# Kernel tuning notes

Measured on AMD Instinct MI355X. Metric: run time of the kernel, lower is better.

## Reference

```python
import jax, jax.numpy as jnp
import numpy as np

D_MODEL = 1024
N_HEADS = 16
D_EXP = 4
B, SQ, SKV = 2, 2048, 2048
LN_EPS = 1e-5


def _linear_params(key, d_in, d_out):
    kw, kb = jax.random.split(key)
    w = jax.random.normal(kw, (d_in, d_out), jnp.float32) * 0.02  # stored [in,out]
    b = jax.random.normal(kb, (d_out,), jnp.float32) * 0.02
    return w, b


def setup_inputs() -> dict:
    key = jax.random.key(0)
    ks = jax.random.split(key, 16)
    inp = {}
    inp["x"] = jax.random.normal(ks[0], (B, SQ, D_MODEL), jnp.float32)
    inp["encoder_out"] = jax.random.normal(ks[1], (B, SKV, D_MODEL), jnp.float32)
    # causal target mask, broadcast over batch and heads
    inp["tgt_mask"] = jnp.tril(jnp.ones((SQ, SQ), jnp.int32))[None, None]
    inp["src_mask"] = jnp.ones((1, 1, SQ, SKV), jnp.int32)
    # self-attention params
    inp["wq_s"], inp["bq_s"] = _linear_params(ks[2], D_MODEL, D_MODEL)
    inp["wk_s"], inp["bk_s"] = _linear_params(ks[3], D_MODEL, D_MODEL)
    inp["wv_s"], inp["bv_s"] = _linear_params(ks[4], D_MODEL, D_MODEL)
    inp["wo_s"], inp["bo_s"] = _linear_params(ks[5], D_MODEL, D_MODEL)
    # cross-attention params
    inp["wq_c"], inp["bq_c"] = _linear_params(ks[6], D_MODEL, D_MODEL)
    inp["wk_c"], inp["bk_c"] = _linear_params(ks[7], D_MODEL, D_MODEL)
    inp["wv_c"], inp["bv_c"] = _linear_params(ks[8], D_MODEL, D_MODEL)
    inp["wo_c"], inp["bo_c"] = _linear_params(ks[9], D_MODEL, D_MODEL)
    # feedforward params
    inp["ff1_w"], inp["ff1_b"] = _linear_params(ks[10], D_MODEL, D_MODEL * D_EXP)
    inp["ff2_w"], inp["ff2_b"] = _linear_params(ks[11], D_MODEL * D_EXP, D_MODEL)
    # layernorm params (3 AddNorms)
    for i, k in zip((1, 2, 3), (ks[12], ks[13], ks[14])):
        inp[f"ln{i}_g"] = jnp.ones((D_MODEL,), jnp.float32)
        inp[f"ln{i}_b"] = jnp.zeros((D_MODEL,), jnp.float32)
    return inp


def _layernorm(x, g, b):
    mu = jnp.mean(x, axis=-1, keepdims=True)
    var = jnp.mean(jnp.square(x - mu), axis=-1, keepdims=True)
    return (x - mu) / jnp.sqrt(var + LN_EPS) * g + b


def _mha(xq, xkv, wq, bq, wk, bk, wv, bv, wo, bo, mask):
    Bq, Sq, D = xq.shape
    Hd = D // N_HEADS
    q = (xq @ wq + bq).reshape(Bq, Sq, N_HEADS, Hd).transpose(0, 2, 1, 3)   # bhqd
    k = (xkv @ wk + bk).reshape(Bq, -1, N_HEADS, Hd).transpose(0, 2, 1, 3)  # bhkd
    v = (xkv @ wv + bv).reshape(Bq, -1, N_HEADS, Hd).transpose(0, 2, 1, 3)  # bhkd
    score = jnp.einsum("bhqd,bhkd->bhqk", q, k) / jnp.sqrt(jnp.float32(Hd))
    score = jnp.where(mask == 0, -jnp.inf, score)
    attn = jax.nn.softmax(score, axis=-1)
    ctx = jnp.einsum("bhqk,bhkd->bhqd", attn, v)
    ctx = ctx.transpose(0, 2, 1, 3).reshape(Bq, Sq, D)
    return ctx @ wo + bo


def reference(x, encoder_out, tgt_mask, src_mask,
              wq_s, bq_s, wk_s, bk_s, wv_s, bv_s, wo_s, bo_s,
              wq_c, bq_c, wk_c, bk_c, wv_c, bv_c, wo_c, bo_c,
              ff1_w, ff1_b, ff2_w, ff2_b,
              ln1_g, ln1_b, ln2_g, ln2_b, ln3_g, ln3_b):
    # dropout is identity in eval mode
    sa = _mha(x, x, wq_s, bq_s, wk_s, bk_s, wv_s, bv_s, wo_s, bo_s, tgt_mask)
    h = _layernorm(x + sa, ln1_g, ln1_b)
    ca = _mha(h, encoder_out, wq_c, bq_c, wk_c, bk_c, wv_c, bv_c, wo_c, bo_c, src_mask)
    h2 = _layernorm(h + ca, ln2_g, ln2_b)
    ff = jax.nn.relu(h2 @ ff1_w + ff1_b) @ ff2_w + ff2_b
    return _layernorm(h2 + ff, ln3_g, ln3_b)
```

## Files before the change

kernel.cpp:

```cpp
#include <hip/hip_runtime.h>
#include <stdint.h>

typedef __bf16 bf16;
typedef __attribute__((ext_vector_type(4))) float f32x4;
typedef __attribute__((ext_vector_type(8))) __bf16 bf16x8;
typedef __attribute__((ext_vector_type(4))) __bf16 bf16x4;

#define DM   1024
#define NH   16
#define HDIM 64
#define BB   2
#define SEQ  2048
#define MR   (BB * SEQ)
#define DFF  4096
#define MEG  (1024 * 1024)

__global__ void detect_kernel(const unsigned int* __restrict__ xw,
                              int* __restrict__ flag) {
  int tid = threadIdx.x;
  int bad = 0;
  for (int i = tid; i < 4096; i += 64) {
    unsigned int w = xw[i];
    float flo = __uint_as_float((w & 0xffffu) << 16);
    if (!(fabsf(flo) < 100.f)) bad = 1;
  }
  unsigned long long m = __ballot(bad);
  if (tid == 0) *flag = (m == 0ull) ? 1 : 0;
}

__global__ __launch_bounds__(256) void cvt_big_kernel(
    const void* __restrict__ src, bf16* __restrict__ dst, int n4,
    const int* __restrict__ flag) {
  int i = blockIdx.x * 256 + threadIdx.x;
  if (i >= n4) return;
  if (*flag) {
    ((bf16x4*)dst)[i] = ((const bf16x4*)src)[i];
  } else {
    float4 v = ((const float4*)src)[i];
    bf16x4 o = {(bf16)v.x, (bf16)v.y, (bf16)v.z, (bf16)v.w};
    ((bf16x4*)dst)[i] = o;
  }
}

struct P16 { const void* p[16]; };
__global__ __launch_bounds__(256) void cvt_small_kernel(
    P16 ps, bf16* __restrict__ dstbase, const int* __restrict__ flag) {
  const int ncnt[16] = {1024,1024,1024,1024,1024,1024,1024,1024,
                        4096,1024,1024,1024,1024,1024,1024,1024};
  const int doff[16] = {0,1024,2048,3072,4096,5120,6144,7168,
                        8192,12288,13312,14336,15360,16384,17408,18432};
  int b = blockIdx.x;
  int n = ncnt[b];
  bool isbf = (*flag) != 0;
  const void* s = ps.p[b];
  bf16* d = dstbase + doff[b];
  for (int i = threadIdx.x; i * 4 < n; i += 256) {
    if (isbf) {
      ((bf16x4*)d)[i] = ((const bf16x4*)s)[i];
    } else {
      float4 v = ((const float4*)s)[i];
      bf16x4 o = {(bf16)v.x, (bf16)v.y, (bf16)v.z, (bf16)v.w};
      ((bf16x4*)d)[i] = o;
    }
  }
}

static __device__ __forceinline__ void gl_lds16(const bf16* g, bf16* l) {
  auto gp = reinterpret_cast<__attribute__((address_space(1))) unsigned int*>(
      reinterpret_cast<uintptr_t>(g));
  auto lp = reinterpret_cast<__attribute__((address_space(3))) unsigned int*>(
      (unsigned int)reinterpret_cast<uintptr_t>(l));
  __builtin_amdgcn_global_load_lds(gp, lp, 16, 0, 0);
}

struct WTB {
  const void* src[10];
  int dstoff[10];
  int K[10], N[10];
  int bstart[10];
};
__global__ __launch_bounds__(256) void wt_all_kernel(WTB wb, bf16* __restrict__ wtbase,
                                                     const int* __restrict__ flag) {
  __shared__ bf16 tile[32][33];
  int bid = blockIdx.x;
  int wi = 0;
  while (wi < 9 && bid >= wb.bstart[wi + 1]) ++wi;
  int rel = bid - wb.bstart[wi];
  int N = wb.N[wi], K = wb.K[wi];
  int nb = N >> 5;
  int n0 = (rel % nb) * 32, k0 = (rel / nb) * 32;
  const void* w = wb.src[wi];
  bf16* wt = wtbase + wb.dstoff[wi];
  bool isbf = (*flag) != 0;
  int tid = threadIdx.x;
  int tx = tid & 31, ty = tid >> 5;
#pragma unroll
  for (int i = 0; i < 4; ++i) {
    size_t idx = (size_t)(k0 + ty + i * 8) * N + n0 + tx;
    tile[ty + i * 8][tx] = isbf ? ((const bf16*)w)[idx]
                                : (bf16)(((const float*)w)[idx]);
  }
  __syncthreads();
#pragma unroll
  for (int i = 0; i < 4; ++i)
    wt[(size_t)(n0 + ty + i * 8) * K + k0 + tx] = tile[tx][ty + i * 8];
}

template <int TM>
__global__ __launch_bounds__(256) void gemm_kernel(
    const bf16* __restrict__ A, const bf16* __restrict__ Bt,
    const bf16* __restrict__ bias, bf16* __restrict__ outb,
    int M, int N, int K, int relu) {
  constexpr int NI = TM / 32;
  constexpr int WM = TM / 2;
  constexpr int CA = TM / 64;
  __shared__ alignas(16) bf16 As[TM * 32];
  __shared__ alignas(16) bf16 Bs[128 * 32];
  int tid = threadIdx.x;
  int lane = tid & 63, wv = tid >> 6;
  int quad = lane >> 4, l15 = lane & 15;
  int m0 = blockIdx.y * TM, n0 = blockIdx.x * 128;
  int wm = wv >> 1, wn = wv & 1;

  f32x4 acc[NI][4];
#pragma unroll
  for (int i = 0; i < NI; ++i)
#pragma unroll
    for (int j = 0; j < 4; ++j) acc[i][j] = (f32x4){0.f, 0.f, 0.f, 0.f};

  int sr = lane >> 2, sc = (lane & 3) * 8;
  const bf16* gA[CA];
  bf16* lA[CA];
#pragma unroll
  for (int t = 0; t < CA; ++t) {
    int ch = wv * CA + t;
    gA[t] = A + (size_t)(m0 + ch * 16 + sr) * K + sc;
    lA[t] = As + ch * 512 + lane * 8;
  }
  const bf16* gB0 = Bt + (size_t)(n0 + (wv * 2) * 16 + sr) * K + sc;
  const bf16* gB1 = Bt + (size_t)(n0 + (wv * 2 + 1) * 16 + sr) * K + sc;
  bf16* lB0 = Bs + (wv * 2) * 512 + lane * 8;
  bf16* lB1 = Bs + (wv * 2 + 1) * 512 + lane * 8;

  for (int k0 = 0; k0 < K; k0 += 32) {
#pragma unroll
    for (int t = 0; t < CA; ++t) gl_lds16(gA[t] + k0, lA[t]);
    gl_lds16(gB0 + k0, lB0);
    gl_lds16(gB1 + k0, lB1);
    __syncthreads();
    bf16x8 af[NI], bfr[4];
#pragma unroll
    for (int i = 0; i < NI; ++i)
      af[i] = *(const bf16x8*)(As + (wm * WM + i * 16 + l15) * 32 + quad * 8);
#pragma unroll
    for (int j = 0; j < 4; ++j)
      bfr[j] = *(const bf16x8*)(Bs + (wn * 64 + j * 16 + l15) * 32 + quad * 8);
#pragma unroll
    for (int i = 0; i < NI; ++i)
#pragma unroll
      for (int j = 0; j < 4; ++j)
        acc[i][j] = __builtin_amdgcn_mfma_f32_16x16x32_bf16(af[i], bfr[j],
                                                            acc[i][j], 0, 0, 0);
    __syncthreads();
  }

#pragma unroll
  for (int j = 0; j < 4; ++j) {
    int col = n0 + wn * 64 + j * 16 + l15;
    float bval = (float)bias[col];
#pragma unroll
    for (int i = 0; i < NI; ++i) {
      int rb = m0 + wm * WM + i * 16 + quad * 4;
#pragma unroll
      for (int r = 0; r < 4; ++r) {
        float v = acc[i][j][r] + bval;
        if (relu) v = fmaxf(v, 0.f);
        outb[(size_t)(rb + r) * N + col] = (bf16)v;
      }
    }
  }
}

__global__ __launch_bounds__(256) void gemm_splitk_kernel(
    const bf16* __restrict__ A, const bf16* __restrict__ Bt,
    float* __restrict__ pout, int M, int N, int KC, int Ktot) {
  __shared__ alignas(16) bf16 As[128 * 32];
  __shared__ alignas(16) bf16 Bs[128 * 32];
  int tid = threadIdx.x;
  int lane = tid & 63, wv = tid >> 6;
  int quad = lane >> 4, l15 = lane & 15;
  int m0 = blockIdx.y * 128, n0 = blockIdx.x * 128;
  int wm = wv >> 1, wn = wv & 1;
  int kb = blockIdx.z * KC;
  pout += (size_t)blockIdx.z * M * N;

  f32x4 acc[4][4];
#pragma unroll
  for (int i = 0; i < 4; ++i)
#pragma unroll
    for (int j = 0; j < 4; ++j) acc[i][j] = (f32x4){0.f, 0.f, 0.f, 0.f};

  int sr = lane >> 2, sc = (lane & 3) * 8;
  const bf16* gA0 = A + (size_t)(m0 + (wv * 2) * 16 + sr) * Ktot + sc;
  const bf16* gA1 = A + (size_t)(m0 + (wv * 2 + 1) * 16 + sr) * Ktot + sc;
  const bf16* gB0 = Bt + (size_t)(n0 + (wv * 2) * 16 + sr) * Ktot + sc;
  const bf16* gB1 = Bt + (size_t)(n0 + (wv * 2 + 1) * 16 + sr) * Ktot + sc;
  bf16* lA0 = As + (wv * 2) * 512 + lane * 8;
  bf16* lA1 = As + (wv * 2 + 1) * 512 + lane * 8;
  bf16* lB0 = Bs + (wv * 2) * 512 + lane * 8;
  bf16* lB1 = Bs + (wv * 2 + 1) * 512 + lane * 8;

  for (int k0 = kb; k0 < kb + KC; k0 += 32) {
    gl_lds16(gA0 + k0, lA0);
    gl_lds16(gA1 + k0, lA1);
    gl_lds16(gB0 + k0, lB0);
    gl_lds16(gB1 + k0, lB1);
    __syncthreads();
    bf16x8 af[4], bfr[4];
#pragma unroll
    for (int i = 0; i < 4; ++i)
      af[i] = *(const bf16x8*)(As + (wm * 64 + i * 16 + l15) * 32 + quad * 8);
#pragma unroll
    for (int j = 0; j < 4; ++j)
      bfr[j] = *(const bf16x8*)(Bs + (wn * 64 + j * 16 + l15) * 32 + quad * 8);
#pragma unroll
    for (int i = 0; i < 4; ++i)
#pragma unroll
      for (int j = 0; j < 4; ++j)
        acc[i][j] = __builtin_amdgcn_mfma_f32_16x16x32_bf16(af[i], bfr[j],
                                                            acc[i][j], 0, 0, 0);
    __syncthreads();
  }
#pragma unroll
  for (int j = 0; j < 4; ++j) {
    int col = n0 + wn * 64 + j * 16 + l15;
#pragma unroll
    for (int i = 0; i < 4; ++i) {
      int rb = m0 + wm * 64 + i * 16 + quad * 4;
#pragma unroll
      for (int r = 0; r < 4; ++r)
        pout[(size_t)(rb + r) * N + col] = acc[i][j][r];
    }
  }
}

__global__ __launch_bounds__(256) void vt_pre_kernel(
    const bf16* __restrict__ v, int vstride, bf16* __restrict__ vt, int skv) {
  __shared__ bf16 tile[32][33];
  int tid = threadIdx.x;
  int tx = tid & 31, ty = tid >> 5;
  int kv0 = blockIdx.x * 32, d0 = blockIdx.y * 32;
  int bh = blockIdx.z;
  int b = bh >> 4, h = bh & 15;
  const bf16* src = v + (size_t)b * skv * vstride + h * HDIM;
#pragma unroll
  for (int i = 0; i < 4; ++i)
    tile[ty + i * 8][tx] = src[(size_t)(kv0 + ty + i * 8) * vstride + d0 + tx];
  __syncthreads();
  bf16* dst = vt + ((size_t)bh * HDIM + d0) * skv + kv0;
#pragma unroll
  for (int i = 0; i < 4; ++i)
    dst[(size_t)(ty + i * 8) * skv + tx] = tile[tx][ty + i * 8];
}

__global__ __launch_bounds__(256) void flash4_kernel(
    const bf16* __restrict__ Q, int qstride,
    const bf16* __restrict__ Kk, int kstride,
    const bf16* __restrict__ VT, bf16* __restrict__ ctx, int skv, int causal) {
  __shared__ alignas(16) bf16 Kt[2][64 * 72];
  __shared__ alignas(16) bf16 Vt[2][64 * 72];
  __shared__ alignas(16) bf16 Pt[2][4][32 * 72];
  int tid = threadIdx.x;
  int lane = tid & 63, wv = tid >> 6, quad = lane >> 4, l15 = lane & 15;
  int qb = blockIdx.x, h = blockIdx.y, b = blockIdx.z;
  int q0 = qb * 128;
  int qw = q0 + wv * 32;

  bf16x8 qf[2][2];
  const float qsc = 0.125f * 1.44269504f;
#pragma unroll
  for (int a = 0; a < 2; ++a) {
    const bf16* qp = Q + (size_t)(b * SEQ + qw + a * 16 + l15) * qstride + h * HDIM;
    qf[a][0] = *(const bf16x8*)(qp + quad * 8);
    qf[a][1] = *(const bf16x8*)(qp + 32 + quad * 8);
#pragma unroll
    for (int j = 0; j < 8; ++j) {
      qf[a][0][j] = (bf16)((float)qf[a][0][j] * qsc);
      qf[a][1][j] = (bf16)((float)qf[a][1][j] * qsc);
    }
  }
  bf16x8 onesf;
#pragma unroll
  for (int j = 0; j < 8; ++j) onesf[j] = (l15 == 0) ? (bf16)1.0f : (bf16)0.0f;

  f32x4 o[2][4], oL[2];
#pragma unroll
  for (int a = 0; a < 2; ++a) {
    oL[a] = (f32x4){0.f, 0.f, 0.f, 0.f};
#pragma unroll
    for (int j = 0; j < 4; ++j) o[a][j] = (f32x4){0.f, 0.f, 0.f, 0.f};
  }

  int nch = causal ? (q0 + 128) / 64 : skv / 64;
  int srow = tid >> 2, sseg = (tid & 3) * 16;
  const bf16* kg = Kk + (size_t)b * skv * kstride + (size_t)srow * kstride +
                   h * HDIM + sseg;
  const bf16* vg = VT + ((size_t)(b * NH + h) * HDIM + srow) * skv + sseg;

  bf16x8 k0r = *(const bf16x8*)(kg);
  bf16x8 k1r = *(const bf16x8*)(kg + 8);
  bf16x8 v0r = *(const bf16x8*)(vg);
  bf16x8 v1r = *(const bf16x8*)(vg + 8);

  for (int c = 0; c < nch; ++c) {
    int buf = c & 1;
    int kv0 = c * 64;
    *(bf16x8*)(&Kt[buf][srow * 72 + sseg]) = k0r;
    *(bf16x8*)(&Kt[buf][srow * 72 + sseg + 8]) = k1r;
    *(bf16x8*)(&Vt[buf][srow * 72 + sseg]) = v0r;
    *(bf16x8*)(&Vt[buf][srow * 72 + sseg + 8]) = v1r;
    if (c + 1 < nch) {
      const bf16* kn = kg + (size_t)(kv0 + 64) * kstride;
      const bf16* vn = vg + kv0 + 64;
      k0r = *(const bf16x8*)(kn);
      k1r = *(const bf16x8*)(kn + 8);
      v0r = *(const bf16x8*)(vn);
      v1r = *(const bf16x8*)(vn + 8);
    }
    __syncthreads();

    if (!causal || kv0 <= qw + 31) {
      f32x4 s[2][4];
#pragma unroll
      for (int t = 0; t < 4; ++t) {
        bf16x8 kt0 = *(const bf16x8*)(&Kt[buf][(t * 16 + l15) * 72 + quad * 8]);
        bf16x8 kt1 = *(const bf16x8*)(&Kt[buf][(t * 16 + l15) * 72 + 32 + quad * 8]);
#pragma unroll
        for (int a = 0; a < 2; ++a) {
          f32x4 z = (f32x4){0.f, 0.f, 0.f, 0.f};
          z = __builtin_amdgcn_mfma_f32_16x16x32_bf16(kt0, qf[a][0], z, 0, 0, 0);
          z = __builtin_amdgcn_mfma_f32_16x16x32_bf16(kt1, qf[a][1], z, 0, 0, 0);
          s[a][t] = z;
        }
      }
      if (causal && kv0 + 63 > qw) {
#pragma unroll
        for (int a = 0; a < 2; ++a)
#pragma unroll
          for (int t = 0; t < 4; ++t)
#pragma unroll
            for (int r = 0; r < 4; ++r)
              if (kv0 + t * 16 + quad * 4 + r > qw + a * 16 + l15)
                s[a][t][r] = -1e30f;
      }
#pragma unroll
      for (int a = 0; a < 2; ++a)
#pragma unroll
        for (int t = 0; t < 4; ++t) {
          bf16x4 pk;
#pragma unroll
          for (int r = 0; r < 4; ++r)
            pk[r] = (bf16)exp2f(s[a][t][r] - 5.770780f);
          *(bf16x4*)(&Pt[buf][wv][(a * 16 + l15) * 72 + t * 16 + quad * 4]) = pk;
        }
      __asm__ volatile("s_waitcnt lgkmcnt(0)" ::: "memory");
      bf16x8 pf[2][2];
#pragma unroll
      for (int a = 0; a < 2; ++a) {
        pf[a][0] = *(const bf16x8*)(&Pt[buf][wv][(a * 16 + l15) * 72 + quad * 8]);
        pf[a][1] = *(const bf16x8*)(&Pt[buf][wv][(a * 16 + l15) * 72 + 32 + quad * 8]);
        oL[a] = __builtin_amdgcn_mfma_f32_16x16x32_bf16(pf[a][0], onesf, oL[a], 0, 0, 0);
        oL[a] = __builtin_amdgcn_mfma_f32_16x16x32_bf16(pf[a][1], onesf, oL[a], 0, 0, 0);
      }
#pragma unroll
      for (int j = 0; j < 4; ++j) {
        bf16x8 bv0 = *(const bf16x8*)(&Vt[buf][(j * 16 + l15) * 72 + quad * 8]);
        bf16x8 bv1 = *(const bf16x8*)(&Vt[buf][(j * 16 + l15) * 72 + 32 + quad * 8]);
#pragma unroll
        for (int a = 0; a < 2; ++a) {
          o[a][j] = __builtin_amdgcn_mfma_f32_16x16x32_bf16(pf[a][0], bv0, o[a][j], 0, 0, 0);
          o[a][j] = __builtin_amdgcn_mfma_f32_16x16x32_bf16(pf[a][1], bv1, o[a][j], 0, 0, 0);
        }
      }
    }
  }

#pragma unroll
  for (int a = 0; a < 2; ++a)
#pragma unroll
    for (int r = 0; r < 4; ++r) {
      float l = __shfl(oL[a][r], quad * 16, 64);
      float inv = 1.0f / fmaxf(l, 1e-30f);
      bf16* cp = ctx + (size_t)(b * SEQ + qw + a * 16 + quad * 4 + r) * DM + h * HDIM;
#pragma unroll
      for (int j = 0; j < 4; ++j) cp[j * 16 + l15] = (bf16)(o[a][j][r] * inv);
    }
}

template <int NP>
__global__ __launch_bounds__(256) void addnorm_red_kernel(
    const bf16* __restrict__ res, const float* __restrict__ part,
    const bf16* __restrict__ bias, const bf16* __restrict__ g,
    const bf16* __restrict__ be, bf16* __restrict__ yb,
    void* __restrict__ outAny, const int* __restrict__ flag) {
  int row = blockIdx.x, tid = threadIdx.x;
  float a0 = 0.f, a1 = 0.f, a2 = 0.f, a3 = 0.f;
#pragma unroll
  for (int p = 0; p < NP; ++p) {
    float4 v = ((const float4*)(part + (size_t)p * MR * DM + (size_t)row * DM))[tid];
    a0 += v.x; a1 += v.y; a2 += v.z; a3 += v.w;
  }
  bf16x4 bb = ((const bf16x4*)bias)[tid];
  bf16x4 rr = ((const bf16x4*)(res + (size_t)row * DM))[tid];
  float s0 = (float)rr[0] + a0 + (float)bb[0];
  float s1 = (float)rr[1] + a1 + (float)bb[1];
  float s2 = (float)rr[2] + a2 + (float)bb[2];
  float s3 = (float)rr[3] + a3 + (float)bb[3];
  float sum = s0 + s1 + s2 + s3;
  float sq = s0 * s0 + s1 * s1 + s2 * s2 + s3 * s3;
#pragma unroll
  for (int mk = 32; mk >= 1; mk >>= 1) {
    sum += __shfl_xor(sum, mk, 64);
    sq += __shfl_xor(sq, mk, 64);
  }
  __shared__ float red[8];
  int wvi = tid >> 6, lane = tid & 63;
  if (lane == 0) { red[wvi * 2] = sum; red[wvi * 2 + 1] = sq; }
  __syncthreads();
  sum = red[0] + red[2] + red[4] + red[6];
  sq = red[1] + red[3] + red[5] + red[7];
  float mu = sum * (1.0f / DM);
  float var = sq * (1.0f / DM) - mu * mu;
  float rstd = rsqrtf(var + 1e-5f);
  bf16x4 g4 = ((const bf16x4*)g)[tid];
  bf16x4 b4 = ((const bf16x4*)be)[tid];
  float y0 = (s0 - mu) * rstd * (float)g4[0] + (float)b4[0];
  float y1 = (s1 - mu) * rstd * (float)g4[1] + (float)b4[1];
  float y2 = (s2 - mu) * rstd * (float)g4[2] + (float)b4[2];
  float y3 = (s3 - mu) * rstd * (float)g4[3] + (float)b4[3];
  if (yb) {
    bf16x4 ob = {(bf16)y0, (bf16)y1, (bf16)y2, (bf16)y3};
    ((bf16x4*)(yb + (size_t)row * DM))[tid] = ob;
  }
  if (outAny) {
    if (*flag) {
      bf16x4 ob = {(bf16)y0, (bf16)y1, (bf16)y2, (bf16)y3};
      ((bf16x4*)outAny)[(size_t)row * 256 + tid] = ob;
    } else {
      ((float4*)outAny)[(size_t)row * 256 + tid] = make_float4(y0, y1, y2, y3);
    }
  }
}

extern "C" void kernel_launch(void* const* d_in, const int* in_sizes, int n_in,
                              void* d_out, int out_size, void* d_ws, size_t ws_size,
                              hipStream_t stream) {
  (void)in_sizes; (void)n_in; (void)out_size; (void)ws_size;
  const void* x_raw   = d_in[0];
  const void* enc_raw = d_in[1];

  char* ws = (char*)d_ws;
  size_t off = 0;
  auto alloc = [&](size_t bytes) -> void* {
    void* p = ws + off;
    off += (bytes + 255) & ~(size_t)255;
    return p;
  };
  const size_t SB = (size_t)MR * DM;
  int* flag    = (int*)alloc(256);
  bf16* smallb = (bf16*)alloc(20480 * 2);
  bf16* wt   = (bf16*)alloc((size_t)16 * MEG * 2);
  bf16* xb   = (bf16*)alloc(SB * 2);
  bf16* encb = (bf16*)alloc(SB * 2);
  bf16* vtg  = (bf16*)alloc(SB * 2);
  bf16* ctx  = (bf16*)alloc(SB * 2);
  bf16* hb1  = (bf16*)alloc(SB * 2);
  bf16* hb2  = (bf16*)alloc(SB * 2);
  bf16* qkv  = (bf16*)alloc(SB * 3 * 2);
  bf16* kvc  = (bf16*)alloc(SB * 2 * 2);
  float* part = (float*)alloc(SB * 4 * 4);
  bf16* gbuf = qkv;
  bf16* qc   = xb;

  bf16* b_qkvs = smallb + 0;     bf16* b_os  = smallb + 3072;
  bf16* b_qc   = smallb + 4096;  bf16* b_kvc = smallb + 5120;
  bf16* b_oc   = smallb + 7168;  bf16* b_f1  = smallb + 8192;
  bf16* b_f2   = smallb + 12288;
  bf16* l1g = smallb + 13312; bf16* l1b = smallb + 14336;
  bf16* l2g = smallb + 15360; bf16* l2b = smallb + 16384;
  bf16* l3g = smallb + 17408; bf16* l3b = smallb + 18432;

  detect_kernel<<<1, 64, 0, stream>>>((const unsigned int*)x_raw, flag);
  cvt_big_kernel<<<(int)(SB / 1024), 256, 0, stream>>>(x_raw, xb, (int)(SB / 4), flag);
  cvt_big_kernel<<<(int)(SB / 1024), 256, 0, stream>>>(enc_raw, encb, (int)(SB / 4), flag);
  P16 ps;
  ps.p[0] = d_in[5];  ps.p[1] = d_in[7];  ps.p[2] = d_in[9];  ps.p[3] = d_in[11];
  ps.p[4] = d_in[13]; ps.p[5] = d_in[15]; ps.p[6] = d_in[17]; ps.p[7] = d_in[19];
  ps.p[8] = d_in[21]; ps.p[9] = d_in[23];
  ps.p[10] = d_in[24]; ps.p[11] = d_in[25]; ps.p[12] = d_in[26];
  ps.p[13] = d_in[27]; ps.p[14] = d_in[28]; ps.p[15] = d_in[29];
  cvt_small_kernel<<<16, 256, 0, stream>>>(ps, smallb, flag);

  WTB wb;
  const int wsrc[10] = {4, 6, 8, 10, 12, 14, 16, 18, 20, 22};
  for (int i = 0; i < 10; ++i) {
    wb.src[i] = d_in[wsrc[i]];
    wb.K[i] = 1024; wb.N[i] = 1024;
    wb.dstoff[i] = i * MEG;
    wb.bstart[i] = i * 1024;
  }
  wb.N[8] = 4096;
  wb.K[9] = 4096; wb.dstoff[9] = 12 * MEG;
  wb.bstart[9] = 8192 + 4096;
  wt_all_kernel<<<16384, 256, 0, stream>>>(wb, wt, flag);

  gemm_kernel<128><<<dim3(24, 32), 256, 0, stream>>>(xb, wt, b_qkvs, qkv,
                                                     MR, 3072, DM, 0);
  vt_pre_kernel<<<dim3(SEQ / 32, 2, 32), 256, 0, stream>>>(qkv + 2048, 3072, vtg, SEQ);
  flash4_kernel<<<dim3(SEQ / 128, NH, BB), 256, 0, stream>>>(
      qkv, 3072, qkv + 1024, 3072, vtg, ctx, SEQ, 1);
  gemm_splitk_kernel<<<dim3(8, 32, 2), 256, 0, stream>>>(
      ctx, wt + (size_t)3 * MEG, part, MR, DM, 512, DM);
  addnorm_red_kernel<2><<<MR, 256, 0, stream>>>(xb, part, b_os, l1g, l1b,
                                                hb1, nullptr, flag);
  gemm_kernel<64><<<dim3(8, 64), 256, 0, stream>>>(hb1, wt + (size_t)4 * MEG,
                                                   b_qc, qc, MR, DM, DM, 0);
  gemm_kernel<128><<<dim3(16, 32), 256, 0, stream>>>(encb, wt + (size_t)5 * MEG,
                                                     b_kvc, kvc, MR, 2048, DM, 0);
  vt_pre_kernel<<<dim3(SEQ / 32, 2, 32), 256, 0, stream>>>(kvc + 1024, 2048, vtg, SEQ);
  flash4_kernel<<<dim3(SEQ / 128, NH, BB), 256, 0, stream>>>(
      qc, 1024, kvc, 2048, vtg, ctx, SEQ, 0);
  gemm_splitk_kernel<<<dim3(8, 32, 2), 256, 0, stream>>>(
      ctx, wt + (size_t)7 * MEG, part, MR, DM, 512, DM);
  addnorm_red_kernel<2><<<MR, 256, 0, stream>>>(hb1, part, b_oc, l2g, l2b,
                                                hb2, nullptr, flag);
  gemm_kernel<128><<<dim3(32, 32), 256, 0, stream>>>(hb2, wt + (size_t)8 * MEG,
                                                     b_f1, gbuf, MR, DFF, DM, 1);
  gemm_splitk_kernel<<<dim3(8, 32, 4), 256, 0, stream>>>(
      gbuf, wt + (size_t)12 * MEG, part, MR, DM, 1024, DFF);
  addnorm_red_kernel<4><<<MR, 256, 0, stream>>>(hb2, part, b_f2, l3g, l3b,
                                                nullptr, d_out, flag);
}
```

Before: 655.7 us.

## Fuse prep kernels, batch QKV/KV GEMMs, and restructure flash attention with split-KV warps

Merges the input conversion, small-param conversion and weight transpose into one prep launch. Runs the self-attention QKV and cross-attention KV projections in a single dual GEMM launch and transposes both V tensors in one kernel, using separate V buffers. Rewrites the flash attention kernel so each wave covers 64 queries against half of each 64-wide KV chunk, loads K/V straight into LDS with global_load_lds, and reduces the two KV halves through shared memory at the end. This cuts launch count and raises MFMA work per wave, at the cost of more registers and an added per-chunk barrier with no double buffering.

New measurement: 775.2 us. +18.2%, slower.

```diff
diff --git a/kernel.cpp b/kernel.cpp
--- a/kernel.cpp
+++ b/kernel.cpp
@@ -28,40 +28,72 @@
   if (tid == 0) *flag = (m == 0ull) ? 1 : 0;
 }
 
-__global__ __launch_bounds__(256) void cvt_big_kernel(
-    const void* __restrict__ src, bf16* __restrict__ dst, int n4,
+struct P16 { const void* p[16]; };
+struct WTB {
+  const void* src[10];
+  int dstoff[10];
+  int K[10], N[10];
+  int bstart[10];
+};
+
+__global__ __launch_bounds__(256) void prep_kernel(
+    const void* __restrict__ xr, const void* __restrict__ er,
+    bf16* __restrict__ xb, bf16* __restrict__ encb,
+    P16 ps, bf16* __restrict__ smallb, WTB wb, bf16* __restrict__ wtbase,
     const int* __restrict__ flag) {
-  int i = blockIdx.x * 256 + threadIdx.x;
-  if (i >= n4) return;
-  if (*flag) {
-    ((bf16x4*)dst)[i] = ((const bf16x4*)src)[i];
+  int bid = blockIdx.x, tid = threadIdx.x;
+  bool isbf = (*flag) != 0;
+  if (bid < 8192) {
+    const void* src = bid < 4096 ? xr : er;
+    bf16* dst = bid < 4096 ? xb : encb;
+    int i = (bid & 4095) * 256 + tid;
+    if (isbf) {
+      ((bf16x4*)dst)[i] = ((const bf16x4*)src)[i];
+    } else {
+      float4 v = ((const float4*)src)[i];
+      bf16x4 o = {(bf16)v.x, (bf16)v.y, (bf16)v.z, (bf16)v.w};
+      ((bf16x4*)dst)[i] = o;
+    }
+  } else if (bid < 8208) {
+    const int ncnt[16] = {1024,1024,1024,1024,1024,1024,1024,1024,
+                          4096,1024,1024,1024,1024,1024,1024,1024};
+    const int doff[16] = {0,1024,2048,3072,4096,5120,6144,7168,
+                          8192,12288,13312,14336,15360,16384,17408,18432};
+    int b = bid - 8192;
+    int n = ncnt[b];
+    const void* s = ps.p[b];
+    bf16* d = smallb + doff[b];
+    for (int i = tid; i * 4 < n; i += 256) {
+      if (isbf) {
+        ((bf16x4*)d)[i] = ((const bf16x4*)s)[i];
+      } else {
+        float4 v = ((const float4*)s)[i];
+        bf16x4 o = {(bf16)v.x, (bf16)v.y, (bf16)v.z, (bf16)v.w};
+        ((bf16x4*)d)[i] = o;
+      }
+    }
   } else {
-    float4 v = ((const float4*)src)[i];
-    bf16x4 o = {(bf16)v.x, (bf16)v.y, (bf16)v.z, (bf16)v.w};
-    ((bf16x4*)dst)[i] = o;
-  }
-}
-
-struct P16 { const void* p[16]; };
-__global__ __launch_bounds__(256) void cvt_small_kernel(
-    P16 ps, bf16* __restrict__ dstbase, const int* __restrict__ flag) {
-  const int ncnt[16] = {1024,1024,1024,1024,1024,1024,1024,1024,
-                        4096,1024,1024,1024,1024,1024,1024,1024};
-  const int doff[16] = {0,1024,2048,3072,4096,5120,6144,7168,
-                        8192,12288,13312,14336,15360,16384,17408,18432};
-  int b = blockIdx.x;
-  int n = ncnt[b];
-  bool isbf = (*flag) != 0;
-  const void* s = ps.p[b];
-  bf16* d = dstbase + doff[b];
-  for (int i = threadIdx.x; i * 4 < n; i += 256) {
-    if (isbf) {
-      ((bf16x4*)d)[i] = ((const bf16x4*)s)[i];
-    } else {
-      float4 v = ((const float4*)s)[i];
-      bf16x4 o = {(bf16)v.x, (bf16)v.y, (bf16)v.z, (bf16)v.w};
-      ((bf16x4*)d)[i] = o;
-    }
+    __shared__ bf16 tile[32][33];
+    int bid2 = bid - 8208;
+    int wi = 0;
+    while (wi < 9 && bid2 >= wb.bstart[wi + 1]) ++wi;
+    int rel = bid2 - wb.bstart[wi];
+    int N = wb.N[wi], K = wb.K[wi];
+    int nb = N >> 5;
+    int n0 = (rel % nb) * 32, k0 = (rel / nb) * 32;
+    const void* w = wb.src[wi];
+    bf16* wt = wtbase + wb.dstoff[wi];
+    int tx = tid & 31, ty = tid >> 5;
+#pragma unroll
+    for (int i = 0; i < 4; ++i) {
+      size_t idx = (size_t)(k0 + ty + i * 8) * N + n0 + tx;
+      tile[ty + i * 8][tx] = isbf ? ((const bf16*)w)[idx]
+                                  : (bf16)(((const float*)w)[idx]);
+    }
+    __syncthreads();
+#pragma unroll
+    for (int i = 0; i < 4; ++i)
+      wt[(size_t)(n0 + ty + i * 8) * K + k0 + tx] = tile[tx][ty + i * 8];
   }
 }
 
@@ -73,53 +105,18 @@
   __builtin_amdgcn_global_load_lds(gp, lp, 16, 0, 0);
 }
 
-struct WTB {
-  const void* src[10];
-  int dstoff[10];
-  int K[10], N[10];
-  int bstart[10];
-};
-__global__ __launch_bounds__(256) void wt_all_kernel(WTB wb, bf16* __restrict__ wtbase,
-                                                     const int* __restrict__ flag) {
-  __shared__ bf16 tile[32][33];
-  int bid = blockIdx.x;
-  int wi = 0;
-  while (wi < 9 && bid >= wb.bstart[wi + 1]) ++wi;
-  int rel = bid - wb.bstart[wi];
-  int N = wb.N[wi], K = wb.K[wi];
-  int nb = N >> 5;
-  int n0 = (rel % nb) * 32, k0 = (rel / nb) * 32;
-  const void* w = wb.src[wi];
-  bf16* wt = wtbase + wb.dstoff[wi];
-  bool isbf = (*flag) != 0;
-  int tid = threadIdx.x;
-  int tx = tid & 31, ty = tid >> 5;
-#pragma unroll
-  for (int i = 0; i < 4; ++i) {
-    size_t idx = (size_t)(k0 + ty + i * 8) * N + n0 + tx;
-    tile[ty + i * 8][tx] = isbf ? ((const bf16*)w)[idx]
-                                : (bf16)(((const float*)w)[idx]);
-  }
-  __syncthreads();
-#pragma unroll
-  for (int i = 0; i < 4; ++i)
-    wt[(size_t)(n0 + ty + i * 8) * K + k0 + tx] = tile[tx][ty + i * 8];
-}
-
 template <int TM>
-__global__ __launch_bounds__(256) void gemm_kernel(
-    const bf16* __restrict__ A, const bf16* __restrict__ Bt,
+__device__ __forceinline__ void gemm_dev(
+    bf16* As, bf16* Bs, const bf16* __restrict__ A, const bf16* __restrict__ Bt,
     const bf16* __restrict__ bias, bf16* __restrict__ outb,
-    int M, int N, int K, int relu) {
+    int N, int K, int relu, int bx, int by) {
   constexpr int NI = TM / 32;
   constexpr int WM = TM / 2;
   constexpr int CA = TM / 64;
-  __shared__ alignas(16) bf16 As[TM * 32];
-  __shared__ alignas(16) bf16 Bs[128 * 32];
   int tid = threadIdx.x;
   int lane = tid & 63, wv = tid >> 6;
   int quad = lane >> 4, l15 = lane & 15;
-  int m0 = blockIdx.y * TM, n0 = blockIdx.x * 128;
+  int m0 = by * TM, n0 = bx * 128;
   int wm = wv >> 1, wn = wv & 1;
 
   f32x4 acc[NI][4];
@@ -179,6 +176,36 @@
       }
     }
   }
+}
+
+__global__ __launch_bounds__(256) void gemm128_kernel(
+    const bf16* A, const bf16* Bt, const bf16* bias, bf16* outb,
+    int N, int K, int relu) {
+  __shared__ alignas(16) bf16 As[128 * 32];
+  __shared__ alignas(16) bf16 Bs[128 * 32];
+  gemm_dev<128>(As, Bs, A, Bt, bias, outb, N, K, relu, blockIdx.x, blockIdx.y);
+}
+
+__global__ __launch_bounds__(256) void gemm64_kernel(
+    const bf16* A, const bf16* Bt, const bf16* bias, bf16* outb,
+    int N, int K, int relu) {
+  __shared__ alignas(16) bf16 As[64 * 32];
+  __shared__ alignas(16) bf16 Bs[128 * 32];
+  gemm_dev<64>(As, Bs, A, Bt, bias, outb, N, K, relu, blockIdx.x, blockIdx.y);
+}
+
+__global__ __launch_bounds__(256) void gemm_dual_kernel(
+    const bf16* A0, const bf16* B0, const bf16* c0, bf16* o0, int N0, int nb0,
+    const bf16* A1, const bf16* B1, const bf16* c1, bf16* o1, int N1, int K) {
+  __shared__ alignas(16) bf16 As[128 * 32];
+  __shared__ alignas(16) bf16 Bs[128 * 32];
+  int bx = blockIdx.x;
+  const bf16 *A, *Bt, *bias;
+  bf16* outb;
+  int N, bxr;
+  if (bx < nb0) { A = A0; Bt = B0; bias = c0; outb = o0; N = N0; bxr = bx; }
+  else          { A = A1; Bt = B1; bias = c1; outb = o1; N = N1; bxr = bx - nb0; }
+  gemm_dev<128>(As, Bs, A, Bt, bias, outb, N, K, 0, bxr, blockIdx.y);
 }
 
 __global__ __launch_bounds__(256) void gemm_splitk_kernel(
@@ -244,42 +271,51 @@
   }
 }
 
-__global__ __launch_bounds__(256) void vt_pre_kernel(
-    const bf16* __restrict__ v, int vstride, bf16* __restrict__ vt, int skv) {
+__global__ __launch_bounds__(256) void vt_both_kernel(
+    const bf16* __restrict__ vs, int ss, const bf16* __restrict__ vc, int sc2,
+    bf16* __restrict__ vts, bf16* __restrict__ vtc, int skv) {
   __shared__ bf16 tile[32][33];
+  int z = blockIdx.z;
+  int sel = z >> 5, zz = z & 31;
+  const bf16* v = sel ? vc : vs;
+  int vstride = sel ? sc2 : ss;
+  bf16* vt = sel ? vtc : vts;
   int tid = threadIdx.x;
   int tx = tid & 31, ty = tid >> 5;
   int kv0 = blockIdx.x * 32, d0 = blockIdx.y * 32;
-  int bh = blockIdx.z;
-  int b = bh >> 4, h = bh & 15;
+  int b = zz >> 4, h = zz & 15;
   const bf16* src = v + (size_t)b * skv * vstride + h * HDIM;
 #pragma unroll
   for (int i = 0; i < 4; ++i)
     tile[ty + i * 8][tx] = src[(size_t)(kv0 + ty + i * 8) * vstride + d0 + tx];
   __syncthreads();
-  bf16* dst = vt + ((size_t)bh * HDIM + d0) * skv + kv0;
+  bf16* dst = vt + ((size_t)(b * NH + h) * HDIM + d0) * skv + kv0;
 #pragma unroll
   for (int i = 0; i < 4; ++i)
     dst[(size_t)(ty + i * 8) * skv + tx] = tile[tx][ty + i * 8];
 }
 
-__global__ __launch_bounds__(256) void flash4_kernel(
+__global__ __launch_bounds__(256) void flash6_kernel(
     const bf16* __restrict__ Q, int qstride,
     const bf16* __restrict__ Kk, int kstride,
     const bf16* __restrict__ VT, bf16* __restrict__ ctx, int skv, int causal) {
-  __shared__ alignas(16) bf16 Kt[2][64 * 72];
-  __shared__ alignas(16) bf16 Vt[2][64 * 72];
-  __shared__ alignas(16) bf16 Pt[2][4][32 * 72];
+  __shared__ alignas(16) char smem[40960];
+  bf16* Kt = (bf16*)smem;
+  bf16* Vt = (bf16*)(smem + 8192);
+  bf16* Pt = (bf16*)(smem + 16384);
+  float* mbuf = (float*)smem;
+
   int tid = threadIdx.x;
   int lane = tid & 63, wv = tid >> 6, quad = lane >> 4, l15 = lane & 15;
-  int qb = blockIdx.x, h = blockIdx.y, b = blockIdx.z;
-  int q0 = qb * 128;
-  int qw = q0 + wv * 32;
-
-  bf16x8 qf[2][2];
+  int qh = wv >> 1, kh = wv & 1;
+  int q0 = blockIdx.x * 128, h = blockIdx.y, b = blockIdx.z;
+  int qw = q0 + qh * 64;
+  bf16* Ptw = Pt + wv * 2560;
+
   const float qsc = 0.125f * 1.44269504f;
-#pragma unroll
-  for (int a = 0; a < 2; ++a) {
+  bf16x8 qf[4][2];
+#pragma unroll
+  for (int a = 0; a < 4; ++a) {
     const bf16* qp = Q + (size_t)(b * SEQ + qw + a * 16 + l15) * qstride + h * HDIM;
     qf[a][0] = *(const bf16x8*)(qp + quad * 8);
     qf[a][1] = *(const bf16x8*)(qp + 32 + quad * 8);
@@ -293,108 +329,109 @@
 #pragma unroll
   for (int j = 0; j < 8; ++j) onesf[j] = (l15 == 0) ? (bf16)1.0f : (bf16)0.0f;
 
-  f32x4 o[2][4], oL[2];
-#pragma unroll
-  for (int a = 0; a < 2; ++a) {
+  f32x4 o[4][4], oL[4];
+#pragma unroll
+  for (int a = 0; a < 4; ++a) {
     oL[a] = (f32x4){0.f, 0.f, 0.f, 0.f};
 #pragma unroll
     for (int j = 0; j < 4; ++j) o[a][j] = (f32x4){0.f, 0.f, 0.f, 0.f};
   }
 
   int nch = causal ? (q0 + 128) / 64 : skv / 64;
-  int srow = tid >> 2, sseg = (tid & 3) * 16;
-  const bf16* kg = Kk + (size_t)b * skv * kstride + (size_t)srow * kstride +
-                   h * HDIM + sseg;
-  const bf16* vg = VT + ((size_t)(b * NH + h) * HDIM + srow) * skv + sseg;
-
-  bf16x8 k0r = *(const bf16x8*)(kg);
-  bf16x8 k1r = *(const bf16x8*)(kg + 8);
-  bf16x8 v0r = *(const bf16x8*)(vg);
-  bf16x8 v1r = *(const bf16x8*)(vg + 8);
+  const bf16* kg = Kk + (size_t)b * skv * kstride + h * HDIM;
+  const bf16* vg = VT + (size_t)(b * NH + h) * HDIM * skv;
+  int sl_row = lane >> 2, sl_seg = (lane & 3) * 8;
 
   for (int c = 0; c < nch; ++c) {
-    int buf = c & 1;
     int kv0 = c * 64;
-    *(bf16x8*)(&Kt[buf][srow * 72 + sseg]) = k0r;
-    *(bf16x8*)(&Kt[buf][srow * 72 + sseg + 8]) = k1r;
-    *(bf16x8*)(&Vt[buf][srow * 72 + sseg]) = v0r;
-    *(bf16x8*)(&Vt[buf][srow * 72 + sseg + 8]) = v1r;
-    if (c + 1 < nch) {
-      const bf16* kn = kg + (size_t)(kv0 + 64) * kstride;
-      const bf16* vn = vg + kv0 + 64;
-      k0r = *(const bf16x8*)(kn);
-      k1r = *(const bf16x8*)(kn + 8);
-      v0r = *(const bf16x8*)(vn);
-      v1r = *(const bf16x8*)(vn + 8);
-    }
-    __syncthreads();
-
-    if (!causal || kv0 <= qw + 31) {
-      f32x4 s[2][4];
-#pragma unroll
-      for (int t = 0; t < 4; ++t) {
-        bf16x8 kt0 = *(const bf16x8*)(&Kt[buf][(t * 16 + l15) * 72 + quad * 8]);
-        bf16x8 kt1 = *(const bf16x8*)(&Kt[buf][(t * 16 + l15) * 72 + 32 + quad * 8]);
-#pragma unroll
-        for (int a = 0; a < 2; ++a) {
+#pragma unroll
+    for (int i = 0; i < 4; ++i) {
+      int e = wv * 4 + i;
+      if (e < 8) {
+        int p = (e >> 2) & 1, r0 = (e & 3) * 16;
+        gl_lds16(kg + (size_t)(kv0 + r0 + sl_row) * kstride + p * 32 + sl_seg,
+                 Kt + p * 2048 + r0 * 32 + lane * 8);
+      } else {
+        int e2 = e - 8;
+        int kp = e2 >> 2, r0 = (e2 & 3) * 16;
+        gl_lds16(vg + (size_t)(r0 + sl_row) * skv + kv0 + kp * 32 + sl_seg,
+                 Vt + kp * 2048 + r0 * 32 + lane * 8);
+      }
+    }
+    __syncthreads();
+
+    if (!causal || kv0 + kh * 32 <= qw + 63) {
+      bool diag = causal && (kv0 + kh * 32 + 31 > qw);
+#pragma unroll
+      for (int t = 0; t < 2; ++t) {
+        int kvrow = kh * 32 + t * 16;
+        bf16x8 kt0 = *(const bf16x8*)(Kt + (kvrow + l15) * 32 + quad * 8);
+        bf16x8 kt1 = *(const bf16x8*)(Kt + 2048 + (kvrow + l15) * 32 + quad * 8);
+#pragma unroll
+        for (int a = 0; a < 4; ++a) {
           f32x4 z = (f32x4){0.f, 0.f, 0.f, 0.f};
           z = __builtin_amdgcn_mfma_f32_16x16x32_bf16(kt0, qf[a][0], z, 0, 0, 0);
           z = __builtin_amdgcn_mfma_f32_16x16x32_bf16(kt1, qf[a][1], z, 0, 0, 0);
-          s[a][t] = z;
+          if (diag) {
+            int kvg = kv0 + kvrow + quad * 4;
+            int qg = qw + a * 16 + l15;
+#pragma unroll
+            for (int r = 0; r < 4; ++r)
+              if (kvg + r > qg) z[r] = -1e30f;
+          }
+          bf16x4 pk;
+#pragma unroll
+          for (int r = 0; r < 4; ++r) pk[r] = (bf16)exp2f(z[r] - 5.770780f);
+          *(bf16x4*)(Ptw + (a * 16 + l15) * 40 + t * 16 + quad * 4) = pk;
         }
       }
-      if (causal && kv0 + 63 > qw) {
-#pragma unroll
-        for (int a = 0; a < 2; ++a)
-#pragma unroll
-          for (int t = 0; t < 4; ++t)
-#pragma unroll
-            for (int r = 0; r < 4; ++r)
-              if (kv0 + t * 16 + quad * 4 + r > qw + a * 16 + l15)
-                s[a][t][r] = -1e30f;
-      }
-#pragma unroll
-      for (int a = 0; a < 2; ++a)
-#pragma unroll
-        for (int t = 0; t < 4; ++t) {
-          bf16x4 pk;
-#pragma unroll
-          for (int r = 0; r < 4; ++r)
-            pk[r] = (bf16)exp2f(s[a][t][r] - 5.770780f);
-          *(bf16x4*)(&Pt[buf][wv][(a * 16 + l15) * 72 + t * 16 + quad * 4]) = pk;
-        }
       __asm__ volatile("s_waitcnt lgkmcnt(0)" ::: "memory");
-      bf16x8 pf[2][2];
-#pragma unroll
-      for (int a = 0; a < 2; ++a) {
-        pf[a][0] = *(const bf16x8*)(&Pt[buf][wv][(a * 16 + l15) * 72 + quad * 8]);
-        pf[a][1] = *(const bf16x8*)(&Pt[buf][wv][(a * 16 + l15) * 72 + 32 + quad * 8]);
-        oL[a] = __builtin_amdgcn_mfma_f32_16x16x32_bf16(pf[a][0], onesf, oL[a], 0, 0, 0);
-        oL[a] = __builtin_amdgcn_mfma_f32_16x16x32_bf16(pf[a][1], onesf, oL[a], 0, 0, 0);
+      bf16x8 pf[4];
+#pragma unroll
+      for (int a = 0; a < 4; ++a) {
+        pf[a] = *(const bf16x8*)(Ptw + (a * 16 + l15) * 40 + quad * 8);
+        oL[a] = __builtin_amdgcn_mfma_f32_16x16x32_bf16(pf[a], onesf, oL[a], 0, 0, 0);
       }
 #pragma unroll
       for (int j = 0; j < 4; ++j) {
-        bf16x8 bv0 = *(const bf16x8*)(&Vt[buf][(j * 16 + l15) * 72 + quad * 8]);
-        bf16x8 bv1 = *(const bf16x8*)(&Vt[buf][(j * 16 + l15) * 72 + 32 + quad * 8]);
-#pragma unroll
-        for (int a = 0; a < 2; ++a) {
-          o[a][j] = __builtin_amdgcn_mfma_f32_16x16x32_bf16(pf[a][0], bv0, o[a][j], 0, 0, 0);
-          o[a][j] = __builtin_amdgcn_mfma_f32_16x16x32_bf16(pf[a][1], bv1, o[a][j], 0, 0, 0);
-        }
-      }
-    }
-  }
-
-#pragma unroll
-  for (int a = 0; a < 2; ++a)
-#pragma unroll
-    for (int r = 0; r < 4; ++r) {
-      float l = __shfl(oL[a][r], quad * 16, 64);
-      float inv = 1.0f / fmaxf(l, 1e-30f);
-      bf16* cp = ctx + (size_t)(b * SEQ + qw + a * 16 + quad * 4 + r) * DM + h * HDIM;
-#pragma unroll
-      for (int j = 0; j < 4; ++j) cp[j * 16 + l15] = (bf16)(o[a][j][r] * inv);
-    }
+        bf16x8 bv = *(const bf16x8*)(Vt + kh * 2048 + (j * 16 + l15) * 32 + quad * 8);
+#pragma unroll
+        for (int a = 0; a < 4; ++a)
+          o[a][j] = __builtin_amdgcn_mfma_f32_16x16x32_bf16(pf[a], bv, o[a][j], 0, 0, 0);
+      }
+    }
+    __syncthreads();
+  }
+
+  if (kh == 1) {
+    float* mp = mbuf + (size_t)(qh * 64 + lane) * 80;
+#pragma unroll
+    for (int a = 0; a < 4; ++a) {
+#pragma unroll
+      for (int j = 0; j < 4; ++j) *(f32x4*)(mp + (a * 4 + j) * 4) = o[a][j];
+      *(f32x4*)(mp + 64 + a * 4) = oL[a];
+    }
+  }
+  __syncthreads();
+  if (kh == 0) {
+    const float* mp = mbuf + (size_t)(qh * 64 + lane) * 80;
+#pragma unroll
+    for (int a = 0; a < 4; ++a) {
+#pragma unroll
+      for (int j = 0; j < 4; ++j) o[a][j] += *(const f32x4*)(mp + (a * 4 + j) * 4);
+      oL[a] += *(const f32x4*)(mp + 64 + a * 4);
+    }
+#pragma unroll
+    for (int a = 0; a < 4; ++a)
+#pragma unroll
+      for (int r = 0; r < 4; ++r) {
+        float l = __shfl(oL[a][r], quad * 16, 64);
+        float inv = 1.0f / fmaxf(l, 1e-30f);
+        bf16* cp = ctx + (size_t)(b * SEQ + qw + a * 16 + quad * 4 + r) * DM + h * HDIM;
+#pragma unroll
+        for (int j = 0; j < 4; ++j) cp[j * 16 + l15] = (bf16)(o[a][j][r] * inv);
+      }
+  }
 }
 
 template <int NP>
@@ -469,15 +506,16 @@
   const size_t SB = (size_t)MR * DM;
   int* flag    = (int*)alloc(256);
   bf16* smallb = (bf16*)alloc(20480 * 2);
-  bf16* wt   = (bf16*)alloc((size_t)16 * MEG * 2);
-  bf16* xb   = (bf16*)alloc(SB * 2);
-  bf16* encb = (bf16*)alloc(SB * 2);
-  bf16* vtg  = (bf16*)alloc(SB * 2);
-  bf16* ctx  = (bf16*)alloc(SB * 2);
-  bf16* hb1  = (bf16*)alloc(SB * 2);
-  bf16* hb2  = (bf16*)alloc(SB * 2);
-  bf16* qkv  = (bf16*)alloc(SB * 3 * 2);
-  bf16* kvc  = (bf16*)alloc(SB * 2 * 2);
+  bf16* wt    = (bf16*)alloc((size_t)16 * MEG * 2);
+  bf16* xb    = (bf16*)alloc(SB * 2);
+  bf16* encb  = (bf16*)alloc(SB * 2);
+  bf16* vtg_s = (bf16*)alloc(SB * 2);
+  bf16* vtg_c = (bf16*)alloc(SB * 2);
+  bf16* ctx   = (bf16*)alloc(SB * 2);
+  bf16* hb1   = (bf16*)alloc(SB * 2);
+  bf16* hb2   = (bf16*)alloc(SB * 2);
+  bf16* qkv   = (bf16*)alloc(SB * 3 * 2);
+  bf16* kvc   = (bf16*)alloc(SB * 2 * 2);
   float* part = (float*)alloc(SB * 4 * 4);
   bf16* gbuf = qkv;
   bf16* qc   = xb;
@@ -490,16 +528,12 @@
   bf16* l2g = smallb + 15360; bf16* l2b = smallb + 16384;
   bf16* l3g = smallb + 17408; bf16* l3b = smallb + 18432;
 
-  detect_kernel<<<1, 64, 0, stream>>>((const unsigned int*)x_raw, flag);
-  cvt_big_kernel<<<(int)(SB / 1024), 256, 0, stream>>>(x_raw, xb, (int)(SB / 4), flag);
-  cvt_big_kernel<<<(int)(SB / 1024), 256, 0, stream>>>(enc_raw, encb, (int)(SB / 4), flag);
   P16 ps;
   ps.p[0] = d_in[5];  ps.p[1] = d_in[7];  ps.p[2] = d_in[9];  ps.p[3] = d_in[11];
   ps.p[4] = d_in[13]; ps.p[5] = d_in[15]; ps.p[6] = d_in[17]; ps.p[7] = d_in[19];
   ps.p[8] = d_in[21]; ps.p[9] = d_in[23];
   ps.p[10] = d_in[24]; ps.p[11] = d_in[25]; ps.p[12] = d_in[26];
   ps.p[13] = d_in[27]; ps.p[14] = d_in[28]; ps.p[15] = d_in[29];
-  cvt_small_kernel<<<16, 256, 0, stream>>>(ps, smallb, flag);
 
   WTB wb;
   const int wsrc[10] = {4, 6, 8, 10, 12, 14, 16, 18, 20, 22};
@@ -512,30 +546,33 @@
   wb.N[8] = 4096;
   wb.K[9] = 4096; wb.dstoff[9] = 12 * MEG;
   wb.bstart[9] = 8192 + 4096;
-  wt_all_kernel<<<16384, 256, 0, stream>>>(wb, wt, flag);
-
-  gemm_kernel<128><<<dim3(24, 32), 256, 0, stream>>>(xb, wt, b_qkvs, qkv,
-                                                     MR, 3072, DM, 0);
-  vt_pre_kernel<<<dim3(SEQ / 32, 2, 32), 256, 0, stream>>>(qkv + 2048, 3072, vtg, SEQ);
-  flash4_kernel<<<dim3(SEQ / 128, NH, BB), 256, 0, stream>>>(
-      qkv, 3072, qkv + 1024, 3072, vtg, ctx, SEQ, 1);
+
+  detect_kernel<<<1, 64, 0, stream>>>((const unsigned int*)x_raw, flag);
+  prep_kernel<<<24592, 256, 0, stream>>>(x_raw, enc_raw, xb, encb, ps, smallb,
+                                         wb, wt, flag);
+
+  gemm_dual_kernel<<<dim3(40, 32), 256, 0, stream>>>(
+      xb, wt, b_qkvs, qkv, 3072, 24,
+      encb, wt + (size_t)5 * MEG, b_kvc, kvc, 2048, DM);
+  vt_both_kernel<<<dim3(SEQ / 32, 2, 64), 256, 0, stream>>>(
+      qkv + 2048, 3072, kvc + 1024, 2048, vtg_s, vtg_c, SEQ);
+
+  flash6_kernel<<<dim3(SEQ / 128, NH, BB), 256, 0, stream>>>(
+      qkv, 3072, qkv + 1024, 3072, vtg_s, ctx, SEQ, 1);
   gemm_splitk_kernel<<<dim3(8, 32, 2), 256, 0, stream>>>(
       ctx, wt + (size_t)3 * MEG, part, MR, DM, 512, DM);
   addnorm_red_kernel<2><<<MR, 256, 0, stream>>>(xb, part, b_os, l1g, l1b,
                                                 hb1, nullptr, flag);
-  gemm_kernel<64><<<dim3(8, 64), 256, 0, stream>>>(hb1, wt + (size_t)4 * MEG,
-                                                   b_qc, qc, MR, DM, DM, 0);
-  gemm_kernel<128><<<dim3(16, 32), 256, 0, stream>>>(encb, wt + (size_t)5 * MEG,
-                                                     b_kvc, kvc, MR, 2048, DM, 0);
-  vt_pre_kernel<<<dim3(SEQ / 32, 2, 32), 256, 0, stream>>>(kvc + 1024, 2048, vtg, SEQ);
-  flash4_kernel<<<dim3(SEQ / 128, NH, BB), 256, 0, stream>>>(
-      qc, 1024, kvc, 2048, vtg, ctx, SEQ, 0);
+  gemm64_kernel<<<dim3(8, 64), 256, 0, stream>>>(hb1, wt + (size_t)4 * MEG,
+                                                 b_qc, qc, DM, DM, 0);
+  flash6_kernel<<<dim3(SEQ / 128, NH, BB), 256, 0, stream>>>(
+      qc, 1024, kvc, 2048, vtg_c, ctx, SEQ, 0);
   gemm_splitk_kernel<<<dim3(8, 32, 2), 256, 0, stream>>>(
       ctx, wt + (size_t)7 * MEG, part, MR, DM, 512, DM);
   addnorm_red_kernel<2><<<MR, 256, 0, stream>>>(hb1, part, b_oc, l2g, l2b,
                                                 hb2, nullptr, flag);
-  gemm_kernel<128><<<dim3(32, 32), 256, 0, stream>>>(hb2, wt + (size_t)8 * MEG,
-                                                     b_f1, gbuf, MR, DFF, DM, 1);
+  gemm128_kernel<<<dim3(32, 32), 256, 0, stream>>>(hb2, wt + (size_t)8 * MEG,
+                                                   b_f1, gbuf, DFF, DM, 1);
   gemm_splitk_kernel<<<dim3(8, 32, 4), 256, 0, stream>>>(
       gbuf, wt + (size_t)12 * MEG, part, MR, DM, 1024, DFF);
   addnorm_red_kernel<4><<<MR, 256, 0, stream>>>(hb2, part, b_f2, l3g, l3b,
```
